# Kernel optimization log

Measured on AMD Instinct MI355X. Metric: run time of the kernel, lower is better.

The kernel has to match this reference:

```python
import jax, jax.numpy as jnp
import numpy as np

S, N, V, E, H, L = 40, 256, 32000, 1024, 1024, 2


def _gru_step(x, h, wih, whh, bih, bhh):
    # PyTorch GRU cell, gate order [r, z, n]
    gi = x @ wih.T + bih          # (N, 3H)
    gh = h @ whh.T + bhh          # (N, 3H)
    ir, iz, inn = jnp.split(gi, 3, axis=-1)
    hr, hz, hn = jnp.split(gh, 3, axis=-1)
    r = jax.nn.sigmoid(ir + hr)
    z = jax.nn.sigmoid(iz + hz)
    n = jnp.tanh(inn + r * hn)
    return (1.0 - z) * n + z * h


def setup_inputs() -> dict:
    key = jax.random.key(0)
    ks = jax.random.split(key, 16)
    nrm = lambda k, shp: (jax.random.normal(k, shp, jnp.float32) * 0.05)
    return {
        "tokens": jax.random.randint(ks[0], (S, N), 0, V),
        "hidden": jnp.zeros((L, N, H), jnp.float32),
        "emb": nrm(ks[1], (V, E)),
        "enc_wih": nrm(ks[2], (L, 3 * H, E)),
        "enc_whh": nrm(ks[3], (L, 3 * H, H)),
        "enc_bih": nrm(ks[4], (L, 3 * H)),
        "enc_bhh": nrm(ks[5], (L, 3 * H)),
        "dec_wih": nrm(ks[6], (L, 3 * H, H)),
        "dec_whh": nrm(ks[7], (L, 3 * H, H)),
        "dec_bih": nrm(ks[8], (L, 3 * H)),
        "dec_bhh": nrm(ks[9], (L, 3 * H)),
        "attn_w": nrm(ks[10], (S, E + L * H)),
        "attn_b": nrm(ks[11], (S,)),
        "comb_w": nrm(ks[12], (H, 2 * H)),
        "comb_b": nrm(ks[13], (H,)),
    }


def reference(tokens, hidden, emb, enc_wih, enc_whh, enc_bih, enc_bhh,
              dec_wih, dec_whh, dec_bih, dec_bhh,
              attn_w, attn_b, comb_w, comb_b):
    x = emb[tokens]                      # (S, N, E) embedded input

    # ---- encoder: 2-layer GRU over the full sequence ----
    seq = x
    h_finals = []
    for l in range(L):
        wih, whh, bih, bhh = enc_wih[l], enc_whh[l], enc_bih[l], enc_bhh[l]
        def step(h, xt, wih=wih, whh=whh, bih=bih, bhh=bhh):
            h2 = _gru_step(xt, h, wih, whh, bih, bhh)
            return h2, h2
        hT, seq = jax.lax.scan(step, hidden[l], seq)
        h_finals.append(hT)
    h_n = jnp.stack(h_finals)            # (L, N, H)
    enc_out = jnp.swapaxes(seq, 0, 1)    # (N, S, H)

    # ---- attention decoder: scan over timesteps, carry decoder hidden ----
    def dec_step(h, emb_t):
        # h: (L, N, H), emb_t: (N, E)
        h_flat = jnp.swapaxes(h, 0, 1).reshape(N, L * H)
        logits = jnp.concatenate([emb_t, h_flat], axis=-1) @ attn_w.T + attn_b
        aw = jax.nn.softmax(logits, axis=-1)                   # (N, S)
        applied = jnp.einsum('ns,nsh->nh', aw, enc_out)        # (N, H)
        xcur = jax.nn.relu(
            jnp.concatenate([emb_t, applied], axis=-1) @ comb_w.T + comb_b)
        hs = []
        for l in range(L):
            hl = _gru_step(xcur, h[l], dec_wih[l], dec_whh[l],
                           dec_bih[l], dec_bhh[l])
            hs.append(hl)
            xcur = hl
        return jnp.stack(hs), xcur

    hT, outs = jax.lax.scan(dec_step, h_n, x)   # outs: (S, N, H)
    return outs, hT
```

## Files before the change

### kernel.cpp

```cpp
#include <hip/hip_runtime.h>
#include <hip/hip_bf16.h>

#define S_LEN 40
#define NB    256
#define EDIM  1024
#define HDIM  1024
#define NBLK  256
#define NTHR  768

typedef _Float16 f16;
typedef __attribute__((ext_vector_type(8))) _Float16 f16x8;
typedef __attribute__((ext_vector_type(4))) _Float16 f16x4;
typedef __attribute__((ext_vector_type(4))) float f32x4;

__device__ __forceinline__ float sigm(float x) {
    x = fminf(fmaxf(x, -30.f), 30.f);
    return 1.f / (1.f + __expf(-x));
}
__device__ __forceinline__ float tanh_fast(float x) {
    x = fminf(fmaxf(x, -15.f), 15.f);
    float e = __expf(2.f * x);
    return (e - 1.f) / (e + 1.f);
}

__device__ __forceinline__ void sysld_issue_f32(float& v, const void* p) {
    asm volatile("global_load_dword %0, %1, off sc0 sc1" : "=v"(v) : "v"(p));
}
__device__ __forceinline__ void sysld_issue_f32x4(f32x4& v, const void* p) {
    asm volatile("global_load_dwordx4 %0, %1, off sc0 sc1" : "=v"(v) : "v"(p));
}
__device__ __forceinline__ void sys_wait() {
    asm volatile("s_waitcnt vmcnt(0)" ::: "memory");
    __builtin_amdgcn_sched_barrier(0);
}
__device__ __forceinline__ void sysst_f32(float* p, float v) {
    asm volatile("global_store_dword %0, %1, off sc0 sc1" :: "v"(p), "v"(v) : "memory");
}
__device__ __forceinline__ void sysst_f32x4(float* p, f32x4 v) {
    asm volatile("global_store_dwordx4 %0, %1, off sc0 sc1" :: "v"(p), "v"(v) : "memory");
}
__device__ __forceinline__ void sysst_f16(f16* p, f16 v) {
    union { f16 f; unsigned short s; } u; u.f = v;
    unsigned int b = u.s;
    asm volatile("global_store_short %0, %1, off sc0 sc1" :: "v"(p), "v"(b) : "memory");
}

__device__ __forceinline__ void gbar1(unsigned* cnt, unsigned* gen) {
    asm volatile("s_waitcnt vmcnt(0)" ::: "memory");
    __syncthreads();
    if (threadIdx.x == 0) {
        unsigned g = __hip_atomic_load(gen, __ATOMIC_RELAXED, __HIP_MEMORY_SCOPE_AGENT);
        unsigned a = __hip_atomic_fetch_add(cnt, 1u, __ATOMIC_RELEASE, __HIP_MEMORY_SCOPE_AGENT);
        if (a == NBLK - 1) {
            __hip_atomic_store(cnt, 0u, __ATOMIC_RELAXED, __HIP_MEMORY_SCOPE_AGENT);
            __hip_atomic_fetch_add(gen, 1u, __ATOMIC_RELEASE, __HIP_MEMORY_SCOPE_AGENT);
        } else {
            while (__hip_atomic_load(gen, __ATOMIC_RELAXED, __HIP_MEMORY_SCOPE_AGENT) == g)
                __builtin_amdgcn_s_sleep(2);
        }
    }
    __syncthreads();
}

__device__ __forceinline__ void g2bar(unsigned* sync, unsigned xcd,
                                      unsigned M, unsigned NX) {
    asm volatile("s_waitcnt vmcnt(0)" ::: "memory");
    __syncthreads();
    if (threadIdx.x == 0) {
        unsigned* ggen = sync;
        unsigned* gcnt = sync + 1;
        unsigned* xa = sync + 16 + xcd * 16;
        unsigned g = __hip_atomic_load(ggen, __ATOMIC_RELAXED, __HIP_MEMORY_SCOPE_AGENT);
        unsigned a = __hip_atomic_fetch_add(xa, 1u, __ATOMIC_RELEASE, __HIP_MEMORY_SCOPE_AGENT);
        if (a == M - 1) {
            __hip_atomic_store(xa, 0u, __ATOMIC_RELAXED, __HIP_MEMORY_SCOPE_AGENT);
            unsigned b = __hip_atomic_fetch_add(gcnt, 1u, __ATOMIC_RELEASE, __HIP_MEMORY_SCOPE_AGENT);
            if (b == NX - 1) {
                __hip_atomic_store(gcnt, 0u, __ATOMIC_RELAXED, __HIP_MEMORY_SCOPE_AGENT);
                __hip_atomic_fetch_add(ggen, 1u, __ATOMIC_RELEASE, __HIP_MEMORY_SCOPE_AGENT);
            } else {
                while (__hip_atomic_load(ggen, __ATOMIC_RELAXED, __HIP_MEMORY_SCOPE_AGENT) == g)
                    __builtin_amdgcn_s_sleep(4);
            }
        } else {
            while (__hip_atomic_load(ggen, __ATOMIC_RELAXED, __HIP_MEMORY_SCOPE_AGENT) == g)
                __builtin_amdgcn_s_sleep(4);
        }
    }
    __syncthreads();
}

__global__ void k_init_sync(unsigned* s) {
    for (int k = threadIdx.x; k < 1024; k += 256) s[k] = 0;
}

__device__ __forceinline__ void probe_mn(int lane, int* mrow, int* ncol) {
    f16x8 pa, pb;
#pragma unroll
    for (int e = 0; e < 8; e++) {
        pa[e] = (f16)(float)(lane & 15);
        pb[e] = (f16)0.03125f;
    }
    f32x4 pacc = {0, 0, 0, 0};
    pacc = __builtin_amdgcn_mfma_f32_16x16x32_f16(pa, pb, pacc, 0, 0, 0);
#pragma unroll
    for (int r = 0; r < 4; r++) {
        int m = (int)(pacc[r] + 0.5f);
        int cg = ((lane >> 4) << 2) + r;
        mrow[r] = m;
        ncol[r] = (m == cg) ? (lane & 15) : cg;
    }
}

__global__ __launch_bounds__(256) void k_cvt4(const float* __restrict__ src,
                                              f16* __restrict__ dst, int n4) {
    int i = blockIdx.x * 256 + threadIdx.x;
    if (i < n4) {
        f32x4 v = ((const f32x4*)src)[i];
        f16x4 o = {(f16)v.x, (f16)v.y, (f16)v.z, (f16)v.w};
        ((f16x4*)dst)[i] = o;
    }
}
__global__ __launch_bounds__(256) void k_copyf4(const float* __restrict__ src,
                                                float* __restrict__ dst, int n4) {
    int i = blockIdx.x * 256 + threadIdx.x;
    if (i < n4) ((f32x4*)dst)[i] = ((const f32x4*)src)[i];
}
__global__ __launch_bounds__(256) void k_embed_cvt(const int* __restrict__ tok,
                                                   const float* __restrict__ emb,
                                                   f16* __restrict__ xe) {
    int b = blockIdx.x;
    int t = threadIdx.x;
    int token = tok[b];
    f32x4 v = ((const f32x4*)(emb + (size_t)token * EDIM))[t];
    f16x4 o = {(f16)v.x, (f16)v.y, (f16)v.z, (f16)v.w};
    ((f16x4*)(xe + (size_t)b * EDIM))[t] = o;
}

__device__ void gru_phase(
    char* lds, int bid, int tid, const int* mr, const int* nc,
    const f16* __restrict__ xsrc,
    const f16* __restrict__ hsrc, const float* __restrict__ hfsrc,
    const f16* __restrict__ wih, const f16* __restrict__ whh,
    const float* __restrict__ bih, const float* __restrict__ bhh,
    f16* ho16, float* hof, float* o2f) {
    const int cb = (bid & 31) * 32;
    const int rb = (bid >> 5) * 32;

    {
        constexpr int TOT = 8192;
        constexpr int IT = (TOT + NTHR - 1) / NTHR;
        f16x8 val[IT];
#pragma unroll
        for (int i = 0; i < IT; i++) {
            int c = tid + i * NTHR;
            if (c < TOT) {
                int isH = c >> 12;
                int cl = c & 4095;
                int row = cl >> 7, cc = cl & 127;
                const f16* src = (isH ? hsrc : xsrc) +
                                 (size_t)(rb + row) * 1024 + cc * 8;
                val[i] = *(const f16x8*)src;
            }
        }
#pragma unroll
        for (int i = 0; i < IT; i++) {
            int c = tid + i * NTHR;
            if (c < TOT) {
                int isH = c >> 12;
                int cl = c & 4095;
                int row = cl >> 7, cc = cl & 127;
                *(f16x8*)(lds + isH * 65536 + row * 2048 +
                          ((cc ^ (row & 7)) << 4)) = val[i];
            }
        }
    }
    __syncthreads();

    const int w = tid >> 6, lane = tid & 63;
    const int pair = w >> 1, kh = w & 1;
    const int gate = (pair >= 3) ? pair - 3 : pair;
    const int r0 = lane & 15, kk0 = (lane >> 4) * 8;
    const f16* B = ((pair < 3) ? wih : whh) + ((size_t)gate * HDIM + cb) * 1024;
    const f16* B0 = B + (size_t)r0 * 1024 + kk0 + kh * 512;
    const f16* B1 = B + (size_t)(r0 + 16) * 1024 + kk0 + kh * 512;
    const int abase = (pair < 3) ? 0 : 65536;
    const int swz = r0 & 7;
    const char* a0p = lds + abase + r0 * 2048;
    const char* a1p = lds + abase + (r0 + 16) * 2048;

    f32x4 acc00 = {0,0,0,0}, acc01 = {0,0,0,0}, acc10 = {0,0,0,0}, acc11 = {0,0,0,0};
#pragma unroll 4
    for (int k = 0; k < 512; k += 32) {
        int g = (kh * 512 + kk0 + k) >> 3;
        int off = (g ^ swz) << 4;
        f16x8 a0 = *(const f16x8*)(a0p + off);
        f16x8 a1 = *(const f16x8*)(a1p + off);
        f16x8 b0 = *(const f16x8*)(B0 + k);
        f16x8 b1 = *(const f16x8*)(B1 + k);
        acc00 = __builtin_amdgcn_mfma_f32_16x16x32_f16(a0, b0, acc00, 0, 0, 0);
        acc01 = __builtin_amdgcn_mfma_f32_16x16x32_f16(a0, b1, acc01, 0, 0, 0);
        acc10 = __builtin_amdgcn_mfma_f32_16x16x32_f16(a1, b0, acc10, 0, 0, 0);
        acc11 = __builtin_amdgcn_mfma_f32_16x16x32_f16(a1, b1, acc11, 0, 0, 0);
    }
    __syncthreads();

    float* red = (float*)lds;
    float* rw = red + w * 1024;
#pragma unroll
    for (int r = 0; r < 4; r++) {
        rw[mr[r] * 32 + nc[r]]             = acc00[r];
        rw[mr[r] * 32 + nc[r] + 16]        = acc01[r];
        rw[(mr[r] + 16) * 32 + nc[r]]      = acc10[r];
        rw[(mr[r] + 16) * 32 + nc[r] + 16] = acc11[r];
    }
    __syncthreads();

    {
        float hp[2];
#pragma unroll
        for (int it = 0; it < 2; it++) {
            int i = tid + it * NTHR;
            if (i < 1024) {
                int rr = i >> 5, ccn = i & 31;
                sysld_issue_f32(hp[it], hfsrc + (size_t)(rb + rr) * HDIM + cb + ccn);
            }
        }
        sys_wait();
#pragma unroll
        for (int it = 0; it < 2; it++) {
            int i = tid + it * NTHR;
            if (i < 1024) {
                int rr = i >> 5, ccn = i & 31;
                int col = cb + ccn;
                int row = rb + rr;
                float gir = red[i]         + red[1024 + i];
                float giz = red[2048 + i]  + red[3072 + i];
                float gin = red[4096 + i]  + red[5120 + i];
                float ghr = red[6144 + i]  + red[7168 + i];
                float ghz = red[8192 + i]  + red[9216 + i];
                float ghn = red[10240 + i] + red[11264 + i];
                float r = sigm(gir + bih[col] + ghr + bhh[col]);
                float z = sigm(giz + bih[HDIM + col] + ghz + bhh[HDIM + col]);
                float n = tanh_fast(gin + bih[2 * HDIM + col] +
                                    r * (ghn + bhh[2 * HDIM + col]));
                float hn2 = (1.f - z) * n + z * hp[it];
                size_t idx = (size_t)row * HDIM + col;
                sysst_f16(ho16 + idx, (f16)hn2);
                sysst_f32(hof + idx, hn2);
                if (o2f) o2f[idx] = hn2;
            }
        }
    }
}

__device__ void attn_phase(
    char* lds, int bid, int tid,
    const f16* __restrict__ xe_t, const f16* __restrict__ h0,
    const f16* __restrict__ h1,
    const f16* __restrict__ attn_w, const float* __restrict__ attn_b,
    const f16* __restrict__ enc16, f16* __restrict__ appl) {
    float* logit = (float*)(lds + 131072);
    float* awls  = logit + 64;
    const int n = bid;
    const int w = tid >> 6, lane = tid & 63;
    const size_t nrow = (size_t)n * 1024;

    {
        constexpr int TOT = 5504;
        constexpr int IT = (TOT + NTHR - 1) / NTHR;
        f16x8 val[IT];
#pragma unroll
        for (int i = 0; i < IT; i++) {
            int c = tid + i * NTHR;
            if (c < TOT) {
                if (c < 5120) {
                    int s = c >> 7, cc = c & 127;
                    val[i] = *(const f16x8*)(enc16 + ((size_t)s * NB + n) * 1024 + cc * 8);
                } else {
                    int r = c - 5120;
                    const f16* src = (r < 128) ? (xe_t + nrow + r * 8)
                                   : (r < 256) ? (h0 + nrow + (r - 128) * 8)
                                               : (h1 + nrow + (r - 256) * 8);
                    val[i] = *(const f16x8*)src;
                }
            }
        }
#pragma unroll
        for (int i = 0; i < IT; i++) {
            int c = tid + i * NTHR;
            if (c < TOT) {
                if (c < 5120) *(f16x8*)(lds + c * 16) = val[i];
                else          *(f16x8*)(lds + 81920 + (c - 5120) * 16) = val[i];
            }
        }
    }
    __syncthreads();

    if (w < 10) {
#pragma unroll
        for (int si = 0; si < 4; si++) {
            int s = w * 4 + si;
            const f16* wrow = attn_w + (size_t)s * 3072;
            float acc = 0.f;
#pragma unroll
            for (int jj = 0; jj < 6; jj++) {
                int j = lane + jj * 64;
                f16x8 a = *(const f16x8*)(lds + 81920 + j * 16);
                f16x8 b = *(const f16x8*)(wrow + j * 8);
#pragma unroll
                for (int e = 0; e < 8; e++)
                    acc = fmaf((float)a[e], (float)b[e], acc);
            }
            for (int o = 32; o; o >>= 1) acc += __shfl_down(acc, o);
            if (lane == 0) logit[s] = acc + attn_b[s];
        }
    }
    __syncthreads();

    if (w == 0) {
        float v = (lane < S_LEN) ? logit[lane] : -1e30f;
        float m = v;
        for (int o = 32; o; o >>= 1) m = fmaxf(m, __shfl_xor(m, o));
        float e = (lane < S_LEN) ? __expf(v - m) : 0.f;
        float sum = e;
        for (int o = 32; o; o >>= 1) sum += __shfl_xor(sum, o);
        if (lane < S_LEN) awls[lane] = e / sum;
    }
    __syncthreads();

    for (int col = tid; col < 1024; col += NTHR) {
        float acc = 0.f;
#pragma unroll
        for (int s = 0; s < S_LEN; s++)
            acc = fmaf(awls[s], (float)*(const f16*)(lds + s * 2048 + col * 2), acc);
        sysst_f16(appl + (size_t)n * 1024 + col, (f16)acc);
    }
}

__device__ void comb_phase(
    char* lds, int bid, int tid, const int* mr, const int* nc,
    const f16* __restrict__ xe_t, const f16* __restrict__ appl,
    const f16* __restrict__ Bw, const float* __restrict__ bias,
    f16* __restrict__ Cout) {
    const int cb = (bid & 31) * 32;
    const int rb = (bid >> 5) * 32;

    {
        constexpr int TOT = 8192;
        constexpr int IT = (TOT + NTHR - 1) / NTHR;
        f16x8 val[IT];
#pragma unroll
        for (int i = 0; i < IT; i++) {
            int c = tid + i * NTHR;
            if (c < TOT) {
                int row = c >> 8, cc = c & 255;
                const f16* src = (cc < 128)
                    ? (xe_t + (size_t)(rb + row) * 1024 + cc * 8)
                    : (appl + (size_t)(rb + row) * 1024 + (cc - 128) * 8);
                val[i] = *(const f16x8*)src;
            }
        }
#pragma unroll
        for (int i = 0; i < IT; i++) {
            int c = tid + i * NTHR;
            if (c < TOT) {
                int row = c >> 8, cc = c & 255;
                *(f16x8*)(lds + row * 4096 + ((cc ^ (row & 7)) << 4)) = val[i];
            }
        }
    }
    __syncthreads();

    const int w = tid >> 6, lane = tid & 63;
    const int r0 = lane & 15, kk0 = (lane >> 4) * 8;
    const int c0 = (w * 64) / 12, c1 = ((w + 1) * 64) / 12;
    const f16* B0 = Bw + (size_t)(cb + r0) * 2048 + kk0;
    const f16* B1 = Bw + (size_t)(cb + r0 + 16) * 2048 + kk0;
    const int swz = r0 & 7;
    const char* a0p = lds + r0 * 4096;
    const char* a1p = lds + (r0 + 16) * 4096;

    f32x4 acc00 = {0,0,0,0}, acc01 = {0,0,0,0}, acc10 = {0,0,0,0}, acc11 = {0,0,0,0};
    for (int c = c0; c < c1; c++) {
        int g = (c * 32 + kk0) >> 3;
        int off = (g ^ swz) << 4;
        f16x8 a0 = *(const f16x8*)(a0p + off);
        f16x8 a1 = *(const f16x8*)(a1p + off);
        f16x8 b0 = *(const f16x8*)(B0 + c * 32);
        f16x8 b1 = *(const f16x8*)(B1 + c * 32);
        acc00 = __builtin_amdgcn_mfma_f32_16x16x32_f16(a0, b0, acc00, 0, 0, 0);
        acc01 = __builtin_amdgcn_mfma_f32_16x16x32_f16(a0, b1, acc01, 0, 0, 0);
        acc10 = __builtin_amdgcn_mfma_f32_16x16x32_f16(a1, b0, acc10, 0, 0, 0);
        acc11 = __builtin_amdgcn_mfma_f32_16x16x32_f16(a1, b1, acc11, 0, 0, 0);
    }
    __syncthreads();

    float* red = (float*)lds;
    float* rw = red + w * 1024;
#pragma unroll
    for (int r = 0; r < 4; r++) {
        rw[mr[r] * 32 + nc[r]]             = acc00[r];
        rw[mr[r] * 32 + nc[r] + 16]        = acc01[r];
        rw[(mr[r] + 16) * 32 + nc[r]]      = acc10[r];
        rw[(mr[r] + 16) * 32 + nc[r] + 16] = acc11[r];
    }
    __syncthreads();

#pragma unroll
    for (int it = 0; it < 2; it++) {
        int i = tid + it * NTHR;
        if (i < 1024) {
            float s = 0.f;
#pragma unroll
            for (int p = 0; p < 12; p++) s += red[p * 1024 + i];
            int rr = i >> 5, ccn = i & 31;
            s += bias[cb + ccn];
            s = fmaxf(s, 0.f);
            sysst_f16(Cout + (size_t)(rb + rr) * 1024 + cb + ccn, (f16)s);
        }
    }
}

__global__ __launch_bounds__(NTHR, 3) void k_mega(
    const f16* __restrict__ xe,
    f16* H0, f16* H1, float* hf,
    const f16* __restrict__ w_eih, const f16* __restrict__ w_ehh,
    const float* __restrict__ enc_bih, const float* __restrict__ enc_bhh,
    const f16* __restrict__ w_dih, const f16* __restrict__ w_dhh,
    const float* __restrict__ dec_bih, const float* __restrict__ dec_bhh,
    const f16* __restrict__ w_attn, const float* __restrict__ attn_b,
    const f16* __restrict__ w_comb, const float* __restrict__ comb_b,
    f16* XC, f16* AP,
    float* out, unsigned* sync) {
    __shared__ char smem[131584];
    __shared__ unsigned s_meta[4];
    char* lds = smem;
    const int bid = blockIdx.x;
    const int tid = threadIdx.x;
    const int lane = tid & 63;
    const size_t NH = (size_t)NB * HDIM;

    int mr[4], nc[4];
    probe_mn(lane, mr, nc);

    if (tid == 0) {
        unsigned x;
        asm volatile("s_getreg_b32 %0, hwreg(20, 0, 32)" : "=s"(x));
        x &= 7;
        __hip_atomic_fetch_add(sync + 256 + x, 1u,
                               __ATOMIC_RELAXED, __HIP_MEMORY_SCOPE_AGENT);
        s_meta[0] = x;
    }
    __syncthreads();
    gbar1(sync + 512, sync + 513);
    if (tid == 0) {
        unsigned M = __hip_atomic_load(sync + 256 + s_meta[0],
                                       __ATOMIC_RELAXED, __HIP_MEMORY_SCOPE_AGENT);
        unsigned nx = 0;
        for (int i = 0; i < 8; i++)
            nx += (__hip_atomic_load(sync + 256 + i, __ATOMIC_RELAXED,
                                     __HIP_MEMORY_SCOPE_AGENT) > 0) ? 1u : 0u;
        s_meta[2] = M; s_meta[3] = nx;
    }
    __syncthreads();
    const unsigned xcd = s_meta[0], M = s_meta[2], NX = s_meta[3];

    float* h0f[2] = { hf, hf + 2 * NH };
    float* h1f[2] = { hf + NH, hf + 3 * NH };

    for (int t = 0; t < S_LEN; t++) {
        int p = t & 1;
        gru_phase(lds, bid, tid, mr, nc,
                  xe + (size_t)t * NB * EDIM,
                  H0 + (size_t)t * NH, h0f[p],
                  w_eih, w_ehh, enc_bih, enc_bhh,
                  H0 + (size_t)(t + 1) * NH, h0f[p ^ 1], (float*)nullptr);
        g2bar(sync, xcd, M, NX);
        gru_phase(lds, bid, tid, mr, nc,
                  H0 + (size_t)(t + 1) * NH,
                  H1 + (size_t)t * NH, h1f[p],
                  w_eih + (size_t)3 * HDIM * EDIM, w_ehh + (size_t)3 * HDIM * HDIM,
                  enc_bih + 3 * HDIM, enc_bhh + 3 * HDIM,
                  H1 + (size_t)(t + 1) * NH, h1f[p ^ 1], (float*)nullptr);
        g2bar(sync, xcd, M, NX);
    }

    for (int t = 0; t < S_LEN; t++) {
        int g = S_LEN + t;
        int p = g & 1;
        attn_phase(lds, bid, tid,
                   xe + (size_t)t * NB * EDIM,
                   H0 + (size_t)g * NH, H1 + (size_t)g * NH,
                   w_attn, attn_b, H1 + NH, AP + (size_t)t * NH);
        g2bar(sync, xcd, M, NX);
        comb_phase(lds, bid, tid, mr, nc,
                   xe + (size_t)t * NB * EDIM, AP + (size_t)t * NH,
                   w_comb, comb_b, XC + (size_t)t * NH);
        g2bar(sync, xcd, M, NX);
        gru_phase(lds, bid, tid, mr, nc,
                  XC + (size_t)t * NH,
                  H0 + (size_t)g * NH, h0f[p],
                  w_dih, w_dhh, dec_bih, dec_bhh,
                  H0 + (size_t)(g + 1) * NH, h0f[p ^ 1], (float*)nullptr);
        g2bar(sync, xcd, M, NX);
        gru_phase(lds, bid, tid, mr, nc,
                  H0 + (size_t)(g + 1) * NH,
                  H1 + (size_t)g * NH, h1f[p],
                  w_dih + (size_t)3 * HDIM * HDIM, w_dhh + (size_t)3 * HDIM * HDIM,
                  dec_bih + 3 * HDIM, dec_bhh + 3 * HDIM,
                  H1 + (size_t)(g + 1) * NH, h1f[p ^ 1], out + (size_t)t * NH);
        g2bar(sync, xcd, M, NX);
    }

    if (tid < 512) {
        size_t idx = (size_t)bid * 512 + tid;
        f32x4 v;
        sysld_issue_f32x4(v, hf + idx * 4);
        sys_wait();
        sysst_f32x4(out + (size_t)S_LEN * NH + idx * 4, v);
    }
}

extern "C" void kernel_launch(void* const* d_in, const int* in_sizes, int n_in,
                              void* d_out, int out_size, void* d_ws, size_t ws_size,
                              hipStream_t stream) {
    const int*   tokens   = (const int*)d_in[0];
    const float* hidden   = (const float*)d_in[1];
    const float* emb      = (const float*)d_in[2];
    const float* enc_wih  = (const float*)d_in[3];
    const float* enc_whh  = (const float*)d_in[4];
    const float* enc_bih  = (const float*)d_in[5];
    const float* enc_bhh  = (const float*)d_in[6];
    const float* dec_wih  = (const float*)d_in[7];
    const float* dec_whh  = (const float*)d_in[8];
    const float* dec_bih  = (const float*)d_in[9];
    const float* dec_bhh  = (const float*)d_in[10];
    const float* attn_w   = (const float*)d_in[11];
    const float* attn_b   = (const float*)d_in[12];
    const float* comb_w   = (const float*)d_in[13];
    const float* comb_b   = (const float*)d_in[14];
    float* out = (float*)d_out;

    const size_t NH = (size_t)NB * HDIM;
    const size_t WSZ = (size_t)2 * 3 * HDIM * EDIM;

    float* hf = (float*)d_ws;
    f16* wp = (f16*)(hf + 4 * NH);
    f16 *w_eih = wp;  wp += WSZ;
    f16 *w_ehh = wp;  wp += WSZ;
    f16 *w_dih = wp;  wp += WSZ;
    f16 *w_dhh = wp;  wp += WSZ;
    f16 *w_comb = wp; wp += (size_t)HDIM * 2048;
    f16 *w_attn = wp; wp += (size_t)S_LEN * 3072;
    f16 *xe = wp;     wp += (size_t)S_LEN * NB * EDIM;
    f16 *H0 = wp;     wp += (size_t)(2 * S_LEN + 1) * NH;
    f16 *H1 = wp;     wp += (size_t)(2 * S_LEN + 1) * NH;
    f16 *XC = wp;     wp += (size_t)S_LEN * NH;
    f16 *AP = wp;     wp += (size_t)S_LEN * NH;
    unsigned* syncp = (unsigned*)((((uintptr_t)wp) + 255) & ~(uintptr_t)255);

    k_init_sync<<<1, 256, 0, stream>>>(syncp);

    k_cvt4<<<(int)(WSZ / 4 / 256), 256, 0, stream>>>(enc_wih, w_eih, (int)(WSZ / 4));
    k_cvt4<<<(int)(WSZ / 4 / 256), 256, 0, stream>>>(enc_whh, w_ehh, (int)(WSZ / 4));
    k_cvt4<<<(int)(WSZ / 4 / 256), 256, 0, stream>>>(dec_wih, w_dih, (int)(WSZ / 4));
    k_cvt4<<<(int)(WSZ / 4 / 256), 256, 0, stream>>>(dec_whh, w_dhh, (int)(WSZ / 4));
    k_cvt4<<<(int)(HDIM * 2048 / 4 / 256), 256, 0, stream>>>(comb_w, w_comb,
                                                             HDIM * 2048 / 4);
    k_cvt4<<<(S_LEN * 3072 / 4 + 255) / 256, 256, 0, stream>>>(attn_w, w_attn,
                                                               S_LEN * 3072 / 4);
    k_embed_cvt<<<S_LEN * NB, 256, 0, stream>>>(tokens, emb, xe);
    k_cvt4<<<(int)(NH / 4 / 256), 256, 0, stream>>>(hidden, H0, (int)(NH / 4));
    k_cvt4<<<(int)(NH / 4 / 256), 256, 0, stream>>>(hidden + NH, H1, (int)(NH / 4));
    k_copyf4<<<(int)(NH / 4 / 256), 256, 0, stream>>>(hidden, hf, (int)(NH / 4));
    k_copyf4<<<(int)(NH / 4 / 256), 256, 0, stream>>>(hidden + NH, hf + NH, (int)(NH / 4));

    k_mega<<<NBLK, NTHR, 0, stream>>>(
        xe, H0, H1, hf,
        w_eih, w_ehh, enc_bih, enc_bhh,
        w_dih, w_dhh, dec_bih, dec_bhh,
        w_attn, attn_b, w_comb, comb_b,
        XC, AP, out, syncp);
}
```

Baseline: 5.612 ms.

## Drop fp32 hidden-state mirror and read previous hidden from staged LDS fp16

Removes the fp32 copy of the recurrent hidden state kept in global memory with system-coherent loads and stores. The previous hidden value for the GRU update is now read from the fp16 tile already staged in LDS for the matmul, and the final hidden state is written straight to the output on the last step. The encoder loop is also split so layer 0 runs over all timesteps before layer 1, which keeps the same number of barriers. This cuts global traffic and the extra copy kernels, but the blend term now uses fp16-rounded hidden values, which adds some accumulated error.

```diff
diff --git a/kernel.cpp b/kernel.cpp
--- a/kernel.cpp
+++ b/kernel.cpp
@@ -23,22 +23,6 @@
     return (e - 1.f) / (e + 1.f);
 }
 
-__device__ __forceinline__ void sysld_issue_f32(float& v, const void* p) {
-    asm volatile("global_load_dword %0, %1, off sc0 sc1" : "=v"(v) : "v"(p));
-}
-__device__ __forceinline__ void sysld_issue_f32x4(f32x4& v, const void* p) {
-    asm volatile("global_load_dwordx4 %0, %1, off sc0 sc1" : "=v"(v) : "v"(p));
-}
-__device__ __forceinline__ void sys_wait() {
-    asm volatile("s_waitcnt vmcnt(0)" ::: "memory");
-    __builtin_amdgcn_sched_barrier(0);
-}
-__device__ __forceinline__ void sysst_f32(float* p, float v) {
-    asm volatile("global_store_dword %0, %1, off sc0 sc1" :: "v"(p), "v"(v) : "memory");
-}
-__device__ __forceinline__ void sysst_f32x4(float* p, f32x4 v) {
-    asm volatile("global_store_dwordx4 %0, %1, off sc0 sc1" :: "v"(p), "v"(v) : "memory");
-}
 __device__ __forceinline__ void sysst_f16(f16* p, f16 v) {
     union { f16 f; unsigned short s; } u; u.f = v;
     unsigned int b = u.s;
@@ -121,11 +105,6 @@
         ((f16x4*)dst)[i] = o;
     }
 }
-__global__ __launch_bounds__(256) void k_copyf4(const float* __restrict__ src,
-                                                float* __restrict__ dst, int n4) {
-    int i = blockIdx.x * 256 + threadIdx.x;
-    if (i < n4) ((f32x4*)dst)[i] = ((const f32x4*)src)[i];
-}
 __global__ __launch_bounds__(256) void k_embed_cvt(const int* __restrict__ tok,
                                                    const float* __restrict__ emb,
                                                    f16* __restrict__ xe) {
@@ -139,11 +118,10 @@
 
 __device__ void gru_phase(
     char* lds, int bid, int tid, const int* mr, const int* nc,
-    const f16* __restrict__ xsrc,
-    const f16* __restrict__ hsrc, const float* __restrict__ hfsrc,
+    const f16* __restrict__ xsrc, const f16* __restrict__ hsrc,
     const f16* __restrict__ wih, const f16* __restrict__ whh,
     const float* __restrict__ bih, const float* __restrict__ bhh,
-    f16* ho16, float* hof, float* o2f) {
+    f16* ho16, float* of_step, float* of_fin) {
     const int cb = (bid & 31) * 32;
     const int rb = (bid >> 5) * 32;
 
@@ -216,40 +194,31 @@
     }
     __syncthreads();
 
-    {
-        float hp[2];
-#pragma unroll
-        for (int it = 0; it < 2; it++) {
-            int i = tid + it * NTHR;
-            if (i < 1024) {
-                int rr = i >> 5, ccn = i & 31;
-                sysld_issue_f32(hp[it], hfsrc + (size_t)(rb + rr) * HDIM + cb + ccn);
-            }
-        }
-        sys_wait();
-#pragma unroll
-        for (int it = 0; it < 2; it++) {
-            int i = tid + it * NTHR;
-            if (i < 1024) {
-                int rr = i >> 5, ccn = i & 31;
-                int col = cb + ccn;
-                int row = rb + rr;
-                float gir = red[i]         + red[1024 + i];
-                float giz = red[2048 + i]  + red[3072 + i];
-                float gin = red[4096 + i]  + red[5120 + i];
-                float ghr = red[6144 + i]  + red[7168 + i];
-                float ghz = red[8192 + i]  + red[9216 + i];
-                float ghn = red[10240 + i] + red[11264 + i];
-                float r = sigm(gir + bih[col] + ghr + bhh[col]);
-                float z = sigm(giz + bih[HDIM + col] + ghz + bhh[HDIM + col]);
-                float n = tanh_fast(gin + bih[2 * HDIM + col] +
-                                    r * (ghn + bhh[2 * HDIM + col]));
-                float hn2 = (1.f - z) * n + z * hp[it];
-                size_t idx = (size_t)row * HDIM + col;
-                sysst_f16(ho16 + idx, (f16)hn2);
-                sysst_f32(hof + idx, hn2);
-                if (o2f) o2f[idx] = hn2;
-            }
+#pragma unroll
+    for (int it = 0; it < 2; it++) {
+        int i = tid + it * NTHR;
+        if (i < 1024) {
+            int rr = i >> 5, ccn = i & 31;
+            int col = cb + ccn;
+            int row = rb + rr;
+            float gir = red[i]         + red[1024 + i];
+            float giz = red[2048 + i]  + red[3072 + i];
+            float gin = red[4096 + i]  + red[5120 + i];
+            float ghr = red[6144 + i]  + red[7168 + i];
+            float ghz = red[8192 + i]  + red[9216 + i];
+            float ghn = red[10240 + i] + red[11264 + i];
+            float r = sigm(gir + bih[col] + ghr + bhh[col]);
+            float z = sigm(giz + bih[HDIM + col] + ghz + bhh[HDIM + col]);
+            float n = tanh_fast(gin + bih[2 * HDIM + col] +
+                                r * (ghn + bhh[2 * HDIM + col]));
+            int gidx = col >> 3, within = col & 7;
+            float hp = (float)*(const f16*)(lds + 65536 + rr * 2048 +
+                                            ((gidx ^ (rr & 7)) << 4) + within * 2);
+            float hn2 = (1.f - z) * n + z * hp;
+            size_t idx = (size_t)row * HDIM + col;
+            sysst_f16(ho16 + idx, (f16)hn2);
+            if (of_step) of_step[idx] = hn2;
+            if (of_fin)  of_fin[idx] = hn2;
         }
     }
 }
@@ -424,7 +393,7 @@
 
 __global__ __launch_bounds__(NTHR, 3) void k_mega(
     const f16* __restrict__ xe,
-    f16* H0, f16* H1, float* hf,
+    f16* H0, f16* H1,
     const f16* __restrict__ w_eih, const f16* __restrict__ w_ehh,
     const float* __restrict__ enc_bih, const float* __restrict__ enc_bhh,
     const f16* __restrict__ w_dih, const f16* __restrict__ w_dhh,
@@ -466,29 +435,24 @@
     __syncthreads();
     const unsigned xcd = s_meta[0], M = s_meta[2], NX = s_meta[3];
 
-    float* h0f[2] = { hf, hf + 2 * NH };
-    float* h1f[2] = { hf + NH, hf + 3 * NH };
-
     for (int t = 0; t < S_LEN; t++) {
-        int p = t & 1;
         gru_phase(lds, bid, tid, mr, nc,
-                  xe + (size_t)t * NB * EDIM,
-                  H0 + (size_t)t * NH, h0f[p],
+                  xe + (size_t)t * NB * EDIM, H0 + (size_t)t * NH,
                   w_eih, w_ehh, enc_bih, enc_bhh,
-                  H0 + (size_t)(t + 1) * NH, h0f[p ^ 1], (float*)nullptr);
+                  H0 + (size_t)(t + 1) * NH, (float*)nullptr, (float*)nullptr);
         g2bar(sync, xcd, M, NX);
+    }
+    for (int t = 0; t < S_LEN; t++) {
         gru_phase(lds, bid, tid, mr, nc,
-                  H0 + (size_t)(t + 1) * NH,
-                  H1 + (size_t)t * NH, h1f[p],
+                  H0 + (size_t)(t + 1) * NH, H1 + (size_t)t * NH,
                   w_eih + (size_t)3 * HDIM * EDIM, w_ehh + (size_t)3 * HDIM * HDIM,
                   enc_bih + 3 * HDIM, enc_bhh + 3 * HDIM,
-                  H1 + (size_t)(t + 1) * NH, h1f[p ^ 1], (float*)nullptr);
+                  H1 + (size_t)(t + 1) * NH, (float*)nullptr, (float*)nullptr);
         g2bar(sync, xcd, M, NX);
     }
 
     for (int t = 0; t < S_LEN; t++) {
         int g = S_LEN + t;
-        int p = g & 1;
         attn_phase(lds, bid, tid,
                    xe + (size_t)t * NB * EDIM,
                    H0 + (size_t)g * NH, H1 + (size_t)g * NH,
@@ -499,26 +463,18 @@
                    w_comb, comb_b, XC + (size_t)t * NH);
         g2bar(sync, xcd, M, NX);
         gru_phase(lds, bid, tid, mr, nc,
-                  XC + (size_t)t * NH,
-                  H0 + (size_t)g * NH, h0f[p],
+                  XC + (size_t)t * NH, H0 + (size_t)g * NH,
                   w_dih, w_dhh, dec_bih, dec_bhh,
-                  H0 + (size_t)(g + 1) * NH, h0f[p ^ 1], (float*)nullptr);
+                  H0 + (size_t)(g + 1) * NH, (float*)nullptr,
+                  (t == S_LEN - 1) ? (out + (size_t)S_LEN * NH) : (float*)nullptr);
         g2bar(sync, xcd, M, NX);
         gru_phase(lds, bid, tid, mr, nc,
-                  H0 + (size_t)(g + 1) * NH,
-                  H1 + (size_t)g * NH, h1f[p],
+                  H0 + (size_t)(g + 1) * NH, H1 + (size_t)g * NH,
                   w_dih + (size_t)3 * HDIM * HDIM, w_dhh + (size_t)3 * HDIM * HDIM,
                   dec_bih + 3 * HDIM, dec_bhh + 3 * HDIM,
-                  H1 + (size_t)(g + 1) * NH, h1f[p ^ 1], out + (size_t)t * NH);
+                  H1 + (size_t)(g + 1) * NH, out + (size_t)t * NH,
+                  (t == S_LEN - 1) ? (out + (size_t)(S_LEN + 1) * NH) : (float*)nullptr);
         g2bar(sync, xcd, M, NX);
-    }
-
-    if (tid < 512) {
-        size_t idx = (size_t)bid * 512 + tid;
-        f32x4 v;
-        sysld_issue_f32x4(v, hf + idx * 4);
-        sys_wait();
-        sysst_f32x4(out + (size_t)S_LEN * NH + idx * 4, v);
     }
 }
 
@@ -545,8 +501,7 @@
     const size_t NH = (size_t)NB * HDIM;
     const size_t WSZ = (size_t)2 * 3 * HDIM * EDIM;
 
-    float* hf = (float*)d_ws;
-    f16* wp = (f16*)(hf + 4 * NH);
+    f16* wp = (f16*)d_ws;
     f16 *w_eih = wp;  wp += WSZ;
     f16 *w_ehh = wp;  wp += WSZ;
     f16 *w_dih = wp;  wp += WSZ;
@@ -573,11 +528,9 @@
     k_embed_cvt<<<S_LEN * NB, 256, 0, stream>>>(tokens, emb, xe);
     k_cvt4<<<(int)(NH / 4 / 256), 256, 0, stream>>>(hidden, H0, (int)(NH / 4));
     k_cvt4<<<(int)(NH / 4 / 256), 256, 0, stream>>>(hidden + NH, H1, (int)(NH / 4));
-    k_copyf4<<<(int)(NH / 4 / 256), 256, 0, stream>>>(hidden, hf, (int)(NH / 4));
-    k_copyf4<<<(int)(NH / 4 / 256), 256, 0, stream>>>(hidden + NH, hf + NH, (int)(NH / 4));
 
     k_mega<<<NBLK, NTHR, 0, stream>>>(
-        xe, H0, H1, hf,
+        xe, H0, H1,
         w_eih, w_ehh, enc_bih, enc_bhh,
         w_dih, w_dhh, dec_bih, dec_bhh,
         w_attn, attn_b, w_comb, comb_b,
```

Measured after the change: 5.437 ms. 3.1% less time.
